# Kernel tuning notes

Hardware: AMD Instinct MI355X
Metric: run time of the kernel (lower is better)

## Reference

```python
import jax, jax.numpy as jnp
import numpy as np

EPS = 1e-5

def _layernorm(x, g, b):
    mu = jnp.mean(x, axis=-1, keepdims=True)
    var = jnp.mean(jnp.square(x - mu), axis=-1, keepdims=True)
    return (x - mu) * jax.lax.rsqrt(var + EPS) * g + b

def setup_inputs() -> dict:
    key = jax.random.key(0)
    ks = jax.random.split(key, 5)
    F_, H, D = 1024, 16, 64
    B, N = 4, 2048
    s = lambda k, shp, fan: jax.random.normal(k, shp, jnp.float32) * (fan ** -0.5)
    return {
        "x": jax.random.normal(ks[0], (B, N, F_), jnp.float32),
        "Wq": s(ks[1], (H * D, F_), F_),
        "Wkv": s(ks[2], (2 * H * D, F_), F_),
        "Wo": s(ks[3], (F_, H * D), H * D),
        "ln_g": jnp.ones((F_,), jnp.float32),
        "ln_b": jnp.zeros((F_,), jnp.float32),
        "lnc_g": jnp.ones((F_,), jnp.float32),
        "lnc_b": jnp.zeros((F_,), jnp.float32),
    }

def reference(x, Wq, Wkv, Wo, ln_g, ln_b, lnc_g, lnc_b):
    H, D = 16, 64
    scale = D ** -0.5
    skip = x
    xn = _layernorm(x, ln_g, ln_b)          # query path norm
    cn = _layernorm(x, lnc_g, lnc_b)        # context (self) norm
    B, N, _ = x.shape
    q = jnp.einsum('bnf,ef->bne', xn, Wq)   # [B,N,H*D]
    kv = jnp.einsum('bnf,ef->bne', cn, Wkv) # [B,N,2*H*D]
    k, v = jnp.split(kv, 2, axis=-1)
    tohd = lambda t: t.reshape(B, N, H, D).transpose(0, 2, 1, 3)  # b h n d
    q, k, v = tohd(q), tohd(k), tohd(v)
    sim = jnp.einsum('bhnd,bhmd->bhnm', q, k) * scale
    attn = jax.nn.softmax(sim, axis=-1)
    out = jnp.einsum('bhnm,bhmd->bhnd', attn, v)
    out = out.transpose(0, 2, 1, 3).reshape(B, N, H * D)
    out = jnp.einsum('bne,fe->bnf', out, Wo)
    return skip + out
```

## Files before the change

### kernel.cpp

```cpp
#include <hip/hip_runtime.h>
#include <hip/hip_bf16.h>
#include <stdint.h>

typedef __bf16 bf16;
typedef __bf16 bf16x8 __attribute__((ext_vector_type(8)));
typedef __bf16 bf16x4 __attribute__((ext_vector_type(4)));
typedef float f32x4 __attribute__((ext_vector_type(4)));
typedef unsigned u32x2 __attribute__((ext_vector_type(2)));

#define F_DIM 1024
#define NSEQ  2048
#define NB    4
#define NH    16
#define HD    64
#define MROWS (NB * NSEQ)
#define LOG2E 1.44269504088896340736f

__device__ __forceinline__ void gload_lds16(const void* g, void* l) {
    __builtin_amdgcn_global_load_lds(
        (__attribute__((address_space(1))) void*)g,
        (__attribute__((address_space(3))) void*)l,
        16, 0, 0);
}

__device__ __forceinline__ unsigned lds_addr(const void* p) {
    return (unsigned)(size_t)(__attribute__((address_space(3))) const void*)p;
}

__device__ __forceinline__ float exp2_fast(float x) {
    float r;
    asm("v_exp_f32 %0, %1" : "=v"(r) : "v"(x));
    return r;
}

__device__ __forceinline__ unsigned cvtpk_bf16(float lo, float hi) {
    unsigned r;
    asm("v_cvt_pk_bf16_f32 %0, %1, %2" : "=v"(r) : "v"(lo), "v"(hi));
    return r;
}

__global__ __launch_bounds__(256) void ln2_kernel(
    const float* __restrict__ x,
    const float* __restrict__ g1, const float* __restrict__ b1,
    const float* __restrict__ g2, const float* __restrict__ b2,
    bf16* __restrict__ xn, bf16* __restrict__ cn)
{
    const int row = blockIdx.x;
    const int t = threadIdx.x;
    float4 v = reinterpret_cast<const float4*>(x + (size_t)row * F_DIM)[t];
    float s  = v.x + v.y + v.z + v.w;
    float ss = v.x * v.x + v.y * v.y + v.z * v.z + v.w * v.w;
#pragma unroll
    for (int m = 1; m < 64; m <<= 1) {
        s  += __shfl_xor(s, m);
        ss += __shfl_xor(ss, m);
    }
    __shared__ float red[8];
    const int w = t >> 6;
    if ((t & 63) == 0) { red[w] = s; red[4 + w] = ss; }
    __syncthreads();
    s  = red[0] + red[1] + red[2] + red[3];
    ss = red[4] + red[5] + red[6] + red[7];
    const float mu  = s * (1.0f / F_DIM);
    const float var = fmaxf(ss * (1.0f / F_DIM) - mu * mu, 0.0f);
    const float rs  = rsqrtf(var + 1e-5f);

    float4 G1 = reinterpret_cast<const float4*>(g1)[t];
    float4 B1 = reinterpret_cast<const float4*>(b1)[t];
    float4 G2 = reinterpret_cast<const float4*>(g2)[t];
    float4 B2 = reinterpret_cast<const float4*>(b2)[t];
    const float h0 = (v.x - mu) * rs, h1 = (v.y - mu) * rs;
    const float h2 = (v.z - mu) * rs, h3 = (v.w - mu) * rs;
    bf16x4 o1 = { (bf16)(h0 * G1.x + B1.x), (bf16)(h1 * G1.y + B1.y),
                  (bf16)(h2 * G1.z + B1.z), (bf16)(h3 * G1.w + B1.w) };
    bf16x4 o2 = { (bf16)(h0 * G2.x + B2.x), (bf16)(h1 * G2.y + B2.y),
                  (bf16)(h2 * G2.z + B2.z), (bf16)(h3 * G2.w + B2.w) };
    *reinterpret_cast<bf16x4*>(xn + (size_t)row * F_DIM + t * 4) = o1;
    *reinterpret_cast<bf16x4*>(cn + (size_t)row * F_DIM + t * 4) = o2;
}

__global__ __launch_bounds__(256) void cvt_kernel(
    const float* __restrict__ src, bf16* __restrict__ dst, int n4)
{
    int i = blockIdx.x * 256 + threadIdx.x;
    if (i < n4) {
        float4 v = reinterpret_cast<const float4*>(src)[i];
        bf16x4 o = { (bf16)v.x, (bf16)v.y, (bf16)v.z, (bf16)v.w };
        reinterpret_cast<bf16x4*>(dst)[i] = o;
    }
}

__global__ __launch_bounds__(256, 2) void qkv_gemm(
    const bf16* __restrict__ xn, const bf16* __restrict__ cn,
    const bf16* __restrict__ wq, const bf16* __restrict__ wkv,
    bf16* __restrict__ qb, bf16* __restrict__ kvb, float qscale)
{
    __shared__ bf16 As[128 * 32];
    __shared__ bf16 Bs[128 * 32];
    const int t = threadIdx.x;
    const int lane = t & 63;
    const int w = t >> 6;
    const int wr = w >> 1, wc = w & 1;

    int flat = blockIdx.x;
    flat = (flat & 7) * 192 + (flat >> 3);

    const bf16 *A, *B;
    bf16* C;
    int N, bm, bn;
    float osc;
    if (flat < 512) {
        A = xn; B = wq; C = qb; N = 1024; osc = qscale;
        bm = (flat >> 3) * 128; bn = (flat & 7) * 128;
    } else {
        const int f = flat - 512;
        A = cn; B = wkv; C = kvb; N = 2048; osc = 1.0f;
        bm = (f >> 4) * 128; bn = (f & 15) * 128;
    }

    const int r = lane & 15;
    const int kg = (lane >> 4) * 8;

    f32x4 acc[4][4];
#pragma unroll
    for (int i = 0; i < 4; i++)
#pragma unroll
        for (int j = 0; j < 4; j++) acc[i][j] = (f32x4){0.f, 0.f, 0.f, 0.f};

    const int c0 = t, c1 = 256 + t;
    const size_t aoff0 = (size_t)(bm + (c0 >> 2)) * F_DIM + (c0 & 3) * 8;
    const size_t aoff1 = (size_t)(bm + (c1 >> 2)) * F_DIM + (c1 & 3) * 8;
    const size_t boff0 = (size_t)(bn + (c0 >> 2)) * F_DIM + (c0 & 3) * 8;
    const size_t boff1 = (size_t)(bn + (c1 >> 2)) * F_DIM + (c1 & 3) * 8;
    bf16* lA0 = As + (size_t)(0 * 256 + w * 64) * 8;
    bf16* lA1 = As + (size_t)(1 * 256 + w * 64) * 8;
    bf16* lB0 = Bs + (size_t)(0 * 256 + w * 64) * 8;
    bf16* lB1 = Bs + (size_t)(1 * 256 + w * 64) * 8;

    for (int kt = 0; kt < F_DIM; kt += 32) {
        gload_lds16(A + aoff0 + kt, lA0);
        gload_lds16(A + aoff1 + kt, lA1);
        gload_lds16(B + boff0 + kt, lB0);
        gload_lds16(B + boff1 + kt, lB1);
        __syncthreads();
        bf16x8 af[4], bfr[4];
#pragma unroll
        for (int mi = 0; mi < 4; mi++)
            af[mi] = *(const bf16x8*)(As + (wr * 64 + mi * 16 + r) * 32 + kg);
#pragma unroll
        for (int ni = 0; ni < 4; ni++)
            bfr[ni] = *(const bf16x8*)(Bs + (wc * 64 + ni * 16 + r) * 32 + kg);
#pragma unroll
        for (int mi = 0; mi < 4; mi++)
#pragma unroll
            for (int ni = 0; ni < 4; ni++)
                acc[mi][ni] = __builtin_amdgcn_mfma_f32_16x16x32_bf16(
                    af[mi], bfr[ni], acc[mi][ni], 0, 0, 0);
        __syncthreads();
    }

    const int g = lane >> 4;
#pragma unroll
    for (int mi = 0; mi < 4; mi++) {
#pragma unroll
        for (int ni = 0; ni < 4; ni++) {
            const int col = bn + wc * 64 + ni * 16 + r;
#pragma unroll
            for (int j = 0; j < 4; j++) {
                const int row = bm + wr * 64 + mi * 16 + g * 4 + j;
                C[(size_t)row * N + col] = (bf16)(acc[mi][ni][j] * osc);
            }
        }
    }
}

__global__ __launch_bounds__(256, 2) void o_gemm(
    const bf16* __restrict__ A, const bf16* __restrict__ B,
    float* __restrict__ Cf, const float* __restrict__ skip)
{
    __shared__ bf16 As[128 * 32];
    __shared__ bf16 Bs[128 * 32];
    const int t = threadIdx.x;
    const int lane = t & 63;
    const int w = t >> 6;
    const int wr = w >> 1, wc = w & 1;

    int flat = blockIdx.x;
    flat = (flat & 7) * 64 + (flat >> 3);
    const int bm = (flat >> 3) * 128;
    const int bn = (flat & 7) * 128;

    const int r = lane & 15;
    const int kg = (lane >> 4) * 8;

    f32x4 acc[4][4];
#pragma unroll
    for (int i = 0; i < 4; i++)
#pragma unroll
        for (int j = 0; j < 4; j++) acc[i][j] = (f32x4){0.f, 0.f, 0.f, 0.f};

    const int c0 = t, c1 = 256 + t;
    const size_t aoff0 = (size_t)(bm + (c0 >> 2)) * F_DIM + (c0 & 3) * 8;
    const size_t aoff1 = (size_t)(bm + (c1 >> 2)) * F_DIM + (c1 & 3) * 8;
    const size_t boff0 = (size_t)(bn + (c0 >> 2)) * F_DIM + (c0 & 3) * 8;
    const size_t boff1 = (size_t)(bn + (c1 >> 2)) * F_DIM + (c1 & 3) * 8;
    bf16* lA0 = As + (size_t)(0 * 256 + w * 64) * 8;
    bf16* lA1 = As + (size_t)(1 * 256 + w * 64) * 8;
    bf16* lB0 = Bs + (size_t)(0 * 256 + w * 64) * 8;
    bf16* lB1 = Bs + (size_t)(1 * 256 + w * 64) * 8;

    for (int kt = 0; kt < F_DIM; kt += 32) {
        gload_lds16(A + aoff0 + kt, lA0);
        gload_lds16(A + aoff1 + kt, lA1);
        gload_lds16(B + boff0 + kt, lB0);
        gload_lds16(B + boff1 + kt, lB1);
        __syncthreads();
        bf16x8 af[4], bfr[4];
#pragma unroll
        for (int mi = 0; mi < 4; mi++)
            af[mi] = *(const bf16x8*)(As + (wr * 64 + mi * 16 + r) * 32 + kg);
#pragma unroll
        for (int ni = 0; ni < 4; ni++)
            bfr[ni] = *(const bf16x8*)(Bs + (wc * 64 + ni * 16 + r) * 32 + kg);
#pragma unroll
        for (int mi = 0; mi < 4; mi++)
#pragma unroll
            for (int ni = 0; ni < 4; ni++)
                acc[mi][ni] = __builtin_amdgcn_mfma_f32_16x16x32_bf16(
                    af[mi], bfr[ni], acc[mi][ni], 0, 0, 0);
        __syncthreads();
    }

    const int g = lane >> 4;
#pragma unroll
    for (int mi = 0; mi < 4; mi++) {
#pragma unroll
        for (int ni = 0; ni < 4; ni++) {
            const int col = bn + wc * 64 + ni * 16 + r;
#pragma unroll
            for (int j = 0; j < 4; j++) {
                const int row = bm + wr * 64 + mi * 16 + g * 4 + j;
                Cf[(size_t)row * F_DIM + col] =
                    acc[mi][ni][j] + skip[(size_t)row * F_DIM + col];
            }
        }
    }
}

__global__ __launch_bounds__(512)
__attribute__((amdgpu_waves_per_eu(4, 5)))
void attn_kernel(
    const bf16* __restrict__ q, const bf16* __restrict__ kvp,
    bf16* __restrict__ o)
{
    __shared__ __align__(16) bf16 Ks[128 * 64];
    __shared__ __align__(16) bf16 Vs[128 * 64];
    __shared__ __align__(16) bf16 Ps[8][16 * 72];

    const int bid = blockIdx.x;
    const int idx = (bid & 7) * 128 + (bid >> 3);
    const int bh = idx >> 4;
    const int qt = idx & 15;
    const int b = bh >> 4, h = bh & 15;

    const int t = threadIdx.x, lane = t & 63, w = t >> 6;
    const int r = lane & 15, g = lane >> 4;

    const size_t rowq = (size_t)b * NSEQ;

    size_t ksrc[2], vsrc[2];
#pragma unroll
    for (int c = 0; c < 2; c++) {
        const int p = c * 512 + t;
        const int krow = p >> 3;
        const int kcol = (p & 7) ^ (krow & 7);
        ksrc[c] = (size_t)(rowq + krow) * (2 * F_DIM) + h * HD + kcol * 8;
        const int kvb = p >> 5, dblk = (p >> 3) & 3;
        const int kvl = (p & 7) >> 1, d8 = p & 1;
        vsrc[c] = (size_t)(rowq + kvb * 4 + kvl) * (2 * F_DIM) + F_DIM + h * HD
                  + dblk * 16 + d8 * 8;
    }

    const int q0 = qt * 128 + w * 16;
    bf16x8 qf[2];
#pragma unroll
    for (int kk = 0; kk < 2; kk++)
        qf[kk] = *(const bf16x8*)(q + (rowq + q0 + r) * F_DIM + h * HD + kk * 32 + g * 8);

    f32x4 oacc[4];
#pragma unroll
    for (int i = 0; i < 4; i++) oacc[i] = (f32x4){0.f, 0.f, 0.f, 0.f};
    float m_r = -1e30f, l_r = 0.f;

    const unsigned va    = lds_addr(Vs) + (unsigned)(g * 1024 + r * 8);
    const unsigned pbase = lds_addr(&Ps[w][0]) + (unsigned)((r * 72 + g * 8) * 2);

    for (int kv0 = 0; kv0 < NSEQ; kv0 += 128) {
        asm volatile("s_barrier" ::: "memory");
        const size_t koff = (size_t)kv0 * (2 * F_DIM);
#pragma unroll
        for (int c = 0; c < 2; c++) {
            gload_lds16(kvp + ksrc[c] + koff, Ks + (size_t)(c * 512 + (t & ~63)) * 8);
            gload_lds16(kvp + vsrc[c] + koff, Vs + (size_t)(c * 512 + (t & ~63)) * 8);
        }
        asm volatile("s_waitcnt vmcnt(0)\n\ts_barrier" ::: "memory");

        f32x4 s4[8];
#pragma unroll
        for (int nt = 0; nt < 8; nt++) s4[nt] = (f32x4){0.f, 0.f, 0.f, 0.f};
        __builtin_amdgcn_s_setprio(1);
#pragma unroll
        for (int kk = 0; kk < 2; kk++) {
#pragma unroll
            for (int nt = 0; nt < 8; nt++) {
                const unsigned lb = (unsigned)((nt * 16 + r) * 128 + kk * 64 + g * 16)
                                    ^ (unsigned)((r & 7) << 4);
                bf16x8 kf = *(const bf16x8*)((const char*)Ks + lb);
                s4[nt] = __builtin_amdgcn_mfma_f32_16x16x32_bf16(kf, qf[kk], s4[nt], 0, 0, 0);
            }
        }
        __builtin_amdgcn_s_setprio(0);

        float mx = s4[0][0];
#pragma unroll
        for (int nt = 0; nt < 8; nt++)
#pragma unroll
            for (int j = 0; j < 4; j++) mx = fmaxf(mx, s4[nt][j]);
        mx = fmaxf(mx, __shfl_xor(mx, 16));
        mx = fmaxf(mx, __shfl_xor(mx, 32));
        if (!__all(mx <= m_r + 8.0f)) {
            const float mnew = fmaxf(m_r, mx);
            const float alpha = exp2_fast(m_r - mnew);
            l_r *= alpha;
#pragma unroll
            for (int j = 0; j < 4; j++) {
                const float aj = __shfl(alpha, g * 4 + j);
#pragma unroll
                for (int ntd = 0; ntd < 4; ntd++) oacc[ntd][j] *= aj;
            }
            m_r = mnew;
        }
        u32x2 pa2[8];
        float ps = 0.f;
#pragma unroll
        for (int nt = 0; nt < 8; nt++) {
            const float e0 = exp2_fast(s4[nt][0] - m_r);
            const float e1 = exp2_fast(s4[nt][1] - m_r);
            const float e2 = exp2_fast(s4[nt][2] - m_r);
            const float e3 = exp2_fast(s4[nt][3] - m_r);
            ps += (e0 + e1) + (e2 + e3);
            pa2[nt] = (u32x2){ cvtpk_bf16(e0, e1), cvtpk_bf16(e2, e3) };
        }
        ps += __shfl_xor(ps, 16);
        ps += __shfl_xor(ps, 32);
        l_r += ps;

#pragma unroll
        for (int hh = 0; hh < 2; hh++) {
#pragma unroll
            for (int nt2 = 0; nt2 < 4; nt2++)
                *(u32x2*)&Ps[w][r * 72 + nt2 * 16 + g * 4] = pa2[hh * 4 + nt2];
            asm volatile("s_waitcnt lgkmcnt(0)" ::: "memory");

            bf16x8 pf[2];
            u32x2 vt[2][4][2];
#pragma unroll
            for (int kk2 = 0; kk2 < 2; kk2++) {
                const unsigned pa = pbase + (unsigned)(kk2 * 64);
                asm volatile("ds_read_b128 %0, %1" : "=v"(pf[kk2]) : "v"(pa));
                const int kkg = hh * 2 + kk2;
#pragma unroll
                for (int ntd = 0; ntd < 4; ntd++) {
                    const unsigned a = va + (unsigned)(kkg * 4096 + ntd * 128);
                    asm volatile("ds_read_b64_tr_b16 %0, %2\n\t"
                                 "ds_read_b64_tr_b16 %1, %2 offset:512"
                                 : "=&v"(vt[kk2][ntd][0]), "=&v"(vt[kk2][ntd][1])
                                 : "v"(a));
                }
            }
            asm volatile("s_waitcnt lgkmcnt(0)" ::: "memory");
            __builtin_amdgcn_sched_barrier(0);

            __builtin_amdgcn_s_setprio(1);
#pragma unroll
            for (int kk2 = 0; kk2 < 2; kk2++)
#pragma unroll
                for (int ntd = 0; ntd < 4; ntd++) {
                    union { u32x2 hl[2]; bf16x8 v; } u;
                    u.hl[0] = vt[kk2][ntd][0];
                    u.hl[1] = vt[kk2][ntd][1];
                    oacc[ntd] = __builtin_amdgcn_mfma_f32_16x16x32_bf16(pf[kk2], u.v, oacc[ntd], 0, 0, 0);
                }
            __builtin_amdgcn_s_setprio(0);
        }
    }

    float rl[4];
#pragma unroll
    for (int j = 0; j < 4; j++) {
        const float lj = __shfl(l_r, g * 4 + j);
        rl[j] = 1.0f / lj;
    }
#pragma unroll
    for (int ntd = 0; ntd < 4; ntd++)
#pragma unroll
        for (int j = 0; j < 4; j++) {
            const int row = q0 + g * 4 + j;
            o[(rowq + row) * F_DIM + h * HD + ntd * 16 + r] =
                (bf16)(oacc[ntd][j] * rl[j]);
        }
}

extern "C" void kernel_launch(void* const* d_in, const int* in_sizes, int n_in,
                              void* d_out, int out_size, void* d_ws, size_t ws_size,
                              hipStream_t stream)
{
    const float* x     = (const float*)d_in[0];
    const float* Wq    = (const float*)d_in[1];
    const float* Wkv   = (const float*)d_in[2];
    const float* Wo    = (const float*)d_in[3];
    const float* ln_g  = (const float*)d_in[4];
    const float* ln_b  = (const float*)d_in[5];
    const float* lnc_g = (const float*)d_in[6];
    const float* lnc_b = (const float*)d_in[7];
    float* out = (float*)d_out;

    bf16* xn   = (bf16*)d_ws;
    bf16* cn   = xn  + (size_t)MROWS * F_DIM;
    bf16* qb   = cn  + (size_t)MROWS * F_DIM;
    bf16* kvb  = qb  + (size_t)MROWS * F_DIM;
    bf16* wqb  = kvb + (size_t)MROWS * 2 * F_DIM;
    bf16* wkvb = wqb + (size_t)F_DIM * F_DIM;
    bf16* wob  = wkvb + (size_t)2 * F_DIM * F_DIM;
    bf16* ao   = xn;

    ln2_kernel<<<dim3(MROWS), dim3(256), 0, stream>>>(x, ln_g, ln_b, lnc_g, lnc_b, xn, cn);

    cvt_kernel<<<dim3((F_DIM * F_DIM / 4 + 255) / 256), dim3(256), 0, stream>>>(Wq, wqb, F_DIM * F_DIM / 4);
    cvt_kernel<<<dim3((2 * F_DIM * F_DIM / 4 + 255) / 256), dim3(256), 0, stream>>>(Wkv, wkvb, 2 * F_DIM * F_DIM / 4);
    cvt_kernel<<<dim3((F_DIM * F_DIM / 4 + 255) / 256), dim3(256), 0, stream>>>(Wo, wob, F_DIM * F_DIM / 4);

    qkv_gemm<<<dim3(1536), dim3(256), 0, stream>>>(
        xn, cn, wqb, wkvb, qb, kvb, 0.125f * LOG2E);
    attn_kernel<<<dim3(NSEQ / 128 * NB * NH), dim3(512), 0, stream>>>(qb, kvb, ao);
    o_gemm<<<dim3(512), dim3(256), 0, stream>>>(ao, wob, out, x);
}
```

Measured before the change: 219.7 us.

## Prefetch next K/V tiles into LDS during softmax and PV phases

The attention loop no longer loads K and V, waits for both, and then computes. The next K tile is now issued right after QK^T finishes with the current one, and the next V tile right after PV finishes, with partial vmcnt waits so each load overlaps the other phase's compute. The row-max reduction is also changed to a tree form to shorten the dependency chain. The cost is extra barriers per iteration and more delicate vmcnt ordering, since correctness depends on the global_load_lds completion counts.

```diff
diff --git a/kernel.cpp b/kernel.cpp
--- a/kernel.cpp
+++ b/kernel.cpp
@@ -280,6 +280,10 @@
         vsrc[c] = (size_t)(rowq + kvb * 4 + kvl) * (2 * F_DIM) + F_DIM + h * HD
                   + dblk * 16 + d8 * 8;
     }
+    bf16* kdst0 = Ks + (size_t)(0 * 512 + (t & ~63)) * 8;
+    bf16* kdst1 = Ks + (size_t)(1 * 512 + (t & ~63)) * 8;
+    bf16* vdst0 = Vs + (size_t)(0 * 512 + (t & ~63)) * 8;
+    bf16* vdst1 = Vs + (size_t)(1 * 512 + (t & ~63)) * 8;
 
     const int q0 = qt * 128 + w * 16;
     bf16x8 qf[2];
@@ -295,15 +299,16 @@
     const unsigned va    = lds_addr(Vs) + (unsigned)(g * 1024 + r * 8);
     const unsigned pbase = lds_addr(&Ps[w][0]) + (unsigned)((r * 72 + g * 8) * 2);
 
+    gload_lds16(kvp + ksrc[0], kdst0);
+    gload_lds16(kvp + ksrc[1], kdst1);
+    gload_lds16(kvp + vsrc[0], vdst0);
+    gload_lds16(kvp + vsrc[1], vdst1);
+
     for (int kv0 = 0; kv0 < NSEQ; kv0 += 128) {
-        asm volatile("s_barrier" ::: "memory");
-        const size_t koff = (size_t)kv0 * (2 * F_DIM);
-#pragma unroll
-        for (int c = 0; c < 2; c++) {
-            gload_lds16(kvp + ksrc[c] + koff, Ks + (size_t)(c * 512 + (t & ~63)) * 8);
-            gload_lds16(kvp + vsrc[c] + koff, Vs + (size_t)(c * 512 + (t & ~63)) * 8);
-        }
-        asm volatile("s_waitcnt vmcnt(0)\n\ts_barrier" ::: "memory");
+        const bool more = (kv0 + 128 < NSEQ);
+        const size_t koff = (size_t)(kv0 + 128) * (2 * F_DIM);
+
+        asm volatile("s_waitcnt vmcnt(2)\n\ts_barrier" ::: "memory");
 
         f32x4 s4[8];
 #pragma unroll
@@ -321,11 +326,18 @@
         }
         __builtin_amdgcn_s_setprio(0);
 
-        float mx = s4[0][0];
+        asm volatile("s_barrier" ::: "memory");
+        if (more) {
+            gload_lds16(kvp + ksrc[0] + koff, kdst0);
+            gload_lds16(kvp + ksrc[1] + koff, kdst1);
+        }
+
+        float mnt[8];
 #pragma unroll
         for (int nt = 0; nt < 8; nt++)
-#pragma unroll
-            for (int j = 0; j < 4; j++) mx = fmaxf(mx, s4[nt][j]);
+            mnt[nt] = fmaxf(fmaxf(s4[nt][0], s4[nt][1]), fmaxf(s4[nt][2], s4[nt][3]));
+        float mx = fmaxf(fmaxf(fmaxf(mnt[0], mnt[1]), fmaxf(mnt[2], mnt[3])),
+                         fmaxf(fmaxf(mnt[4], mnt[5]), fmaxf(mnt[6], mnt[7])));
         mx = fmaxf(mx, __shfl_xor(mx, 16));
         mx = fmaxf(mx, __shfl_xor(mx, 32));
         if (!__all(mx <= m_r + 8.0f)) {
@@ -354,6 +366,11 @@
         ps += __shfl_xor(ps, 16);
         ps += __shfl_xor(ps, 32);
         l_r += ps;
+
+        if (more)
+            asm volatile("s_waitcnt vmcnt(2)\n\ts_barrier" ::: "memory");
+        else
+            asm volatile("s_waitcnt vmcnt(0)\n\ts_barrier" ::: "memory");
 
 #pragma unroll
         for (int hh = 0; hh < 2; hh++) {
@@ -393,6 +410,12 @@
                 }
             __builtin_amdgcn_s_setprio(0);
         }
+
+        asm volatile("s_barrier" ::: "memory");
+        if (more) {
+            gload_lds16(kvp + vsrc[0] + koff, vdst0);
+            gload_lds16(kvp + vsrc[1] + koff, vdst1);
+        }
     }
 
     float rl[4];
```

New measurement: 227.1 us. +3.4%, slower.
